# Optimization experiments

Measured on AMD Instinct MI355X. Metric: run time of the kernel, lower is better.

Reference implementation:

```python
import jax, jax.numpy as jnp
import numpy as np


def setup_inputs() -> dict:
    key = jax.random.key(0)
    k1, k2 = jax.random.split(key)
    B, S, D, E = 4, 4096, 2048, 64
    x = jax.random.normal(k1, (B, S, D), dtype=jnp.float32)
    gate_w = jax.random.normal(k2, (E, D), dtype=jnp.float32) * (1.0 / np.sqrt(D))
    return {"x": x, "gate_w": gate_w, "top_k": 2}


def reference(x, gate_w, top_k):
    # logits = x @ W^T : [B, S, E]
    logits = jnp.einsum("bsd,ed->bse", x, gate_w)
    probs = jax.nn.softmax(logits, axis=-1)
    top_k_probs, top_k_indices = jax.lax.top_k(probs, top_k)
    top_k_probs = top_k_probs / jnp.sum(top_k_probs, axis=-1, keepdims=True)
    return (top_k_probs, top_k_indices, probs)
```

## Files before the change

### kernel.cpp

```cpp
#include <hip/hip_runtime.h>
#include <math.h>


typedef _Float16 half8  __attribute__((ext_vector_type(8)));
typedef float    floatx4 __attribute__((ext_vector_type(4)));

#define NTOK  16384
#define DDIM  2048
#define NE    64
#define TPB   64
#define NSTEP 32

__device__ inline void split8(const float4& a, const float4& b,
                              half8& hi, half8& lo) {
    float f[8] = {a.x, a.y, a.z, a.w, b.x, b.y, b.z, b.w};
#pragma unroll
    for (int j = 0; j < 8; ++j) {
        const _Float16 h = (_Float16)f[j];
        hi[j] = h;
        lo[j] = (_Float16)(f[j] - (float)h);
    }
}

__global__ __launch_bounds__(256) void w_split(const float* __restrict__ W,
                                               _Float16* __restrict__ img) {
    const int idx  = blockIdx.x * 256 + threadIdx.x;
    const int step = idx >> 10;
    const int u    = idx & 1023;
    const int hl   = u >> 9;
    const int v    = u & 511;
    const int e    = v >> 3, g = v & 7;
    const float* src = W + (size_t)e * DDIM + step * 64 + 8 * (g ^ (e & 7));
    const float4 a = *(const float4*)(src);
    const float4 b = *(const float4*)(src + 4);
    half8 hi, lo;
    split8(a, b, hi, lo);
    *(half8*)(img + (size_t)idx * 8) = (hl == 0) ? hi : lo;
}

__global__ __launch_bounds__(512) void router_mfma(
    const float* __restrict__ x,
    const _Float16* __restrict__ img,
    float* __restrict__ out)
{
    __shared__ __align__(16) float tiles[16384];
    __shared__ __align__(16) float lg[TPB * 68];

    const int tid = threadIdx.x;
    const int L   = tid & 63;
    const int wv  = __builtin_amdgcn_readfirstlane(tid >> 6);
    const int kh  = wv & 1;
    const int nh  = (wv >> 1) & 1;
    const int mh  = wv >> 2;
    const int c   = L & 15, q = L >> 4;
    const int tok0 = blockIdx.x * TPB;

    const int gfrag = (q + 4 * kh) ^ (L & 7);
    int aoff[2], boff[2];
#pragma unroll
    for (int mt = 0; mt < 2; ++mt)
        aoff[mt] = ((mh * 32 + mt * 16 + c) * 8 + gfrag) * 8;
#pragma unroll
    for (int nt = 0; nt < 2; ++nt)
        boff[nt] = ((nh * 32 + nt * 16 + c) * 8 + gfrag) * 8;

    const int sr = tid >> 3, so = tid & 7;
    const float* xsrc = x + (size_t)(tok0 + sr) * DDIM + 8 * (so ^ (sr & 7));
    const int    xdst = (sr * 8 + so) * 8;
    const float* wsrc = (const float*)img;

    {
        const float4 xa  = *(const float4*)(xsrc);
        const float4 xb  = *(const float4*)(xsrc + 4);
        const float4 wh4 = *(const float4*)(wsrc + (size_t)tid * 4);
        const float4 wl4 = *(const float4*)(wsrc + (size_t)(512 + tid) * 4);
        _Float16* nb = (_Float16*)&tiles[0];
        half8 hi, lo; split8(xa, xb, hi, lo);
        *(half8*)(nb + xdst)        = hi;
        *(half8*)(nb + 4096 + xdst) = lo;
        *(float4*)(nb + 8192  + tid * 8) = wh4;
        *(float4*)(nb + 12288 + tid * 8) = wl4;
    }
    __syncthreads();

    floatx4 acc[2][2];
#pragma unroll
    for (int i = 0; i < 2; ++i)
#pragma unroll
        for (int j = 0; j < 2; ++j) acc[i][j] = (floatx4)0.f;

#pragma unroll 2
    for (int t = 0; t < NSTEP; ++t) {
        float4 xa, xb, wh4, wl4;
        if (t + 1 < NSTEP) {
            xa  = *(const float4*)(xsrc + (t + 1) * 64);
            xb  = *(const float4*)(xsrc + (t + 1) * 64 + 4);
            wh4 = *(const float4*)(wsrc + (size_t)((t + 1) * 1024 + tid) * 4);
            wl4 = *(const float4*)(wsrc + (size_t)((t + 1) * 1024 + 512 + tid) * 4);
        }

        const _Float16* base = (const _Float16*)&tiles[(t & 1) * 8192];
        const _Float16* xh = base;
        const _Float16* xl = base + 4096;
        const _Float16* wh = base + 8192;
        const _Float16* wl = base + 12288;

        half8 Ah[2], Al[2], Bh[2], Bl[2];
#pragma unroll
        for (int mt = 0; mt < 2; ++mt) {
            Ah[mt] = *(const half8*)(xh + aoff[mt]);
            Al[mt] = *(const half8*)(xl + aoff[mt]);
        }
#pragma unroll
        for (int nt = 0; nt < 2; ++nt) {
            Bh[nt] = *(const half8*)(wh + boff[nt]);
            Bl[nt] = *(const half8*)(wl + boff[nt]);
        }
#pragma unroll
        for (int mt = 0; mt < 2; ++mt)
#pragma unroll
            for (int nt = 0; nt < 2; ++nt) {
                acc[mt][nt] = __builtin_amdgcn_mfma_f32_16x16x32_f16(Ah[mt], Bh[nt], acc[mt][nt], 0, 0, 0);
                acc[mt][nt] = __builtin_amdgcn_mfma_f32_16x16x32_f16(Al[mt], Bh[nt], acc[mt][nt], 0, 0, 0);
                acc[mt][nt] = __builtin_amdgcn_mfma_f32_16x16x32_f16(Ah[mt], Bl[nt], acc[mt][nt], 0, 0, 0);
            }

        if (t + 1 < NSTEP) {
            _Float16* nb = (_Float16*)&tiles[((t + 1) & 1) * 8192];
            half8 hi, lo; split8(xa, xb, hi, lo);
            *(half8*)(nb + xdst)        = hi;
            *(half8*)(nb + 4096 + xdst) = lo;
            *(float4*)(nb + 8192  + tid * 8) = wh4;
            *(float4*)(nb + 12288 + tid * 8) = wl4;
        }
        __syncthreads();
    }

    float* exch = tiles;
    const int p = wv >> 1;
    if (kh == 1) {
        float* e0 = &exch[(p * 64 + L) * 20];
        *(float4*)(e0 + 0)  = make_float4(acc[0][0][0], acc[0][0][1], acc[0][0][2], acc[0][0][3]);
        *(float4*)(e0 + 4)  = make_float4(acc[0][1][0], acc[0][1][1], acc[0][1][2], acc[0][1][3]);
        *(float4*)(e0 + 8)  = make_float4(acc[1][0][0], acc[1][0][1], acc[1][0][2], acc[1][0][3]);
        *(float4*)(e0 + 12) = make_float4(acc[1][1][0], acc[1][1][1], acc[1][1][2], acc[1][1][3]);
    }
    __syncthreads();
    if (kh == 0) {
        const float* e0 = &exch[(p * 64 + L) * 20];
        float4 v;
        v = *(const float4*)(e0 + 0);  acc[0][0][0] += v.x; acc[0][0][1] += v.y; acc[0][0][2] += v.z; acc[0][0][3] += v.w;
        v = *(const float4*)(e0 + 4);  acc[0][1][0] += v.x; acc[0][1][1] += v.y; acc[0][1][2] += v.z; acc[0][1][3] += v.w;
        v = *(const float4*)(e0 + 8);  acc[1][0][0] += v.x; acc[1][0][1] += v.y; acc[1][0][2] += v.z; acc[1][0][3] += v.w;
        v = *(const float4*)(e0 + 12); acc[1][1][0] += v.x; acc[1][1][1] += v.y; acc[1][1][2] += v.z; acc[1][1][3] += v.w;
#pragma unroll
        for (int mt = 0; mt < 2; ++mt)
#pragma unroll
            for (int nt = 0; nt < 2; ++nt)
#pragma unroll
                for (int r = 0; r < 4; ++r)
                    lg[(mh * 32 + mt * 16 + q * 4 + r) * 68 + nh * 32 + nt * 16 + c] = acc[mt][nt][r];
    }
    __syncthreads();

    if (tid < 64) {
        const int token = tok0 + tid;
        float* row = &lg[tid * 68];
        float pr[NE];
#pragma unroll
        for (int e = 0; e < NE; ++e) pr[e] = row[e];

        float m = pr[0];
#pragma unroll
        for (int e = 1; e < NE; ++e) m = fmaxf(m, pr[e]);
        float s = 0.f;
#pragma unroll
        for (int e = 0; e < NE; ++e) { pr[e] = expf(pr[e] - m); s += pr[e]; }
        const float inv = 1.f / s;

        float v1 = -1.f; int i1 = 0;
#pragma unroll
        for (int e = 0; e < NE; ++e) { if (pr[e] > v1) { v1 = pr[e]; i1 = e; } }
        float v2 = -1.f; int i2 = 0;
#pragma unroll
        for (int e = 0; e < NE; ++e) { if (e != i1 && pr[e] > v2) { v2 = pr[e]; i2 = e; } }

        const float ts = v1 + v2;
        float* out_tp = out;
        float* out_ti = out + 2 * NTOK;
        *(float2*)(out_tp + token * 2) = make_float2(v1 / ts, v2 / ts);
        *(float2*)(out_ti + token * 2) = make_float2((float)i1, (float)i2);

#pragma unroll
        for (int e = 0; e < NE; ++e) row[e] = pr[e] * inv;
    }
    __syncthreads();

    {
        float* out_p = out + 4 * NTOK + (size_t)tok0 * NE;
#pragma unroll
        for (int i = 0; i < 2; ++i) {
            const int f = tid + 512 * i;
            const int r = f >> 4, c4 = f & 15;
            const float4 v = *(const float4*)&lg[r * 68 + 4 * c4];
            *(float4*)(out_p + f * 4) = v;
        }
    }
}

extern "C" void kernel_launch(void* const* d_in, const int* in_sizes, int n_in,
                              void* d_out, int out_size, void* d_ws, size_t ws_size,
                              hipStream_t stream) {
    const float* x = (const float*)d_in[0];
    const float* W = (const float*)d_in[1];
    float* out     = (float*)d_out;
    _Float16* img  = (_Float16*)d_ws;

    w_split<<<dim3(128), dim3(256), 0, stream>>>(W, img);
    router_mfma<<<dim3(NTOK / TPB), dim3(512), 0, stream>>>(x, img, out);
}
```

Measured before the change: 209.5 us.

## Load MFMA fragments directly from global memory, dropping the LDS staging

The GEMM main loop stops staging x and split W tiles through double-buffered shared memory with a barrier each step. Each wave now loads its x fragments straight from global memory into registers and splits them there. It reads W hi/lo fragments from a new pre-swizzled workspace layout that matches the MFMA operand order, using register double buffering. Blocks shrink to 32 tokens and 256 threads with two waves splitting K, which removes per-step synchronisation but increases register pressure and W re-reads from L2 per block.

New measurement: 226.2 us. 8.0% more time.

```diff
diff --git a/kernel.cpp b/kernel.cpp
--- a/kernel.cpp
+++ b/kernel.cpp
@@ -8,8 +8,6 @@
 #define NTOK  16384
 #define DDIM  2048
 #define NE    64
-#define TPB   64
-#define NSTEP 32
 
 __device__ inline void split8(const float4& a, const float4& b,
                               half8& hi, half8& lo) {
@@ -22,149 +20,110 @@
     }
 }
 
-__global__ __launch_bounds__(256) void w_split(const float* __restrict__ W,
-                                               _Float16* __restrict__ img) {
-    const int idx  = blockIdx.x * 256 + threadIdx.x;
-    const int step = idx >> 10;
-    const int u    = idx & 1023;
-    const int hl   = u >> 9;
-    const int v    = u & 511;
-    const int e    = v >> 3, g = v & 7;
-    const float* src = W + (size_t)e * DDIM + step * 64 + 8 * (g ^ (e & 7));
+__global__ __launch_bounds__(256) void w_split2(const float* __restrict__ W,
+                                                _Float16* __restrict__ img) {
+    const int g  = blockIdx.x * 256 + threadIdx.x;
+    const int L  = g & 63;
+    const int Bk = g >> 6;
+    const int h  = Bk & 1;
+    const int nt = (Bk >> 1) & 3;
+    const int ch = (Bk >> 3) & 1;
+    const int s  = (Bk >> 4) & 15;
+    const int kk = (Bk >> 8) & 1;
+    const int c  = L & 15, q = L >> 4;
+    const float* src = W + (size_t)(nt * 16 + c) * DDIM
+                         + kk * 1024 + s * 64 + ch * 32 + q * 8;
     const float4 a = *(const float4*)(src);
     const float4 b = *(const float4*)(src + 4);
     half8 hi, lo;
     split8(a, b, hi, lo);
-    *(half8*)(img + (size_t)idx * 8) = (hl == 0) ? hi : lo;
+    *(half8*)(img + (size_t)g * 8) = h ? lo : hi;
 }
 
-__global__ __launch_bounds__(512) void router_mfma(
+__global__ __launch_bounds__(256, 2) void router_mfma(
     const float* __restrict__ x,
     const _Float16* __restrict__ img,
     float* __restrict__ out)
 {
-    __shared__ __align__(16) float tiles[16384];
-    __shared__ __align__(16) float lg[TPB * 68];
+    __shared__ __align__(16) float lg[32 * 68];
 
     const int tid = threadIdx.x;
     const int L   = tid & 63;
     const int wv  = __builtin_amdgcn_readfirstlane(tid >> 6);
-    const int kh  = wv & 1;
-    const int nh  = (wv >> 1) & 1;
-    const int mh  = wv >> 2;
+    const int kk  = wv & 1;
+    const int tg  = wv >> 1;
     const int c   = L & 15, q = L >> 4;
-    const int tok0 = blockIdx.x * TPB;
+    const int btok = blockIdx.x * 32;
+    const int tok0 = btok + tg * 16;
 
-    const int gfrag = (q + 4 * kh) ^ (L & 7);
-    int aoff[2], boff[2];
+    const float*    xp = x + (size_t)(tok0 + c) * DDIM + kk * 1024 + q * 8;
+    const _Float16* wp = img + (size_t)kk * 131072 + (size_t)L * 8;
+
+    floatx4 acc[4];
 #pragma unroll
-    for (int mt = 0; mt < 2; ++mt)
-        aoff[mt] = ((mh * 32 + mt * 16 + c) * 8 + gfrag) * 8;
+    for (int nt = 0; nt < 4; ++nt) acc[nt] = (floatx4)0.f;
+
+    float4 xb0[4], xb1[4];
+    half8  wb0[16], wb1[16];
+
+    auto LX = [&](int s, float4* xb) {
 #pragma unroll
-    for (int nt = 0; nt < 2; ++nt)
-        boff[nt] = ((nh * 32 + nt * 16 + c) * 8 + gfrag) * 8;
+        for (int ch = 0; ch < 2; ++ch) {
+            xb[2 * ch + 0] = *(const float4*)(xp + s * 64 + ch * 32);
+            xb[2 * ch + 1] = *(const float4*)(xp + s * 64 + ch * 32 + 4);
+        }
+    };
+    auto LW = [&](int s, half8* wb) {
+#pragma unroll
+        for (int f = 0; f < 16; ++f)
+            wb[f] = *(const half8*)(wp + (size_t)s * 8192 + f * 512);
+    };
+    auto CP = [&](const float4* xb, const half8* wb) {
+#pragma unroll
+        for (int ch = 0; ch < 2; ++ch) {
+            half8 Ah, Al;
+            split8(xb[2 * ch], xb[2 * ch + 1], Ah, Al);
+#pragma unroll
+            for (int nt = 0; nt < 4; ++nt) {
+                const half8 Bh = wb[ch * 8 + nt * 2];
+                const half8 Bl = wb[ch * 8 + nt * 2 + 1];
+                acc[nt] = __builtin_amdgcn_mfma_f32_16x16x32_f16(Ah, Bh, acc[nt], 0, 0, 0);
+                acc[nt] = __builtin_amdgcn_mfma_f32_16x16x32_f16(Al, Bh, acc[nt], 0, 0, 0);
+                acc[nt] = __builtin_amdgcn_mfma_f32_16x16x32_f16(Ah, Bl, acc[nt], 0, 0, 0);
+            }
+        }
+    };
 
-    const int sr = tid >> 3, so = tid & 7;
-    const float* xsrc = x + (size_t)(tok0 + sr) * DDIM + 8 * (so ^ (sr & 7));
-    const int    xdst = (sr * 8 + so) * 8;
-    const float* wsrc = (const float*)img;
+    LX(0, xb0); LW(0, wb0);
+#pragma unroll
+    for (int b = 0; b < 16; b += 2) {
+        LX(b + 1, xb1); LW(b + 1, wb1);
+        CP(xb0, wb0);
+        if (b + 2 < 16) { LX(b + 2, xb0); LW(b + 2, wb0); }
+        CP(xb1, wb1);
+    }
 
-    {
-        const float4 xa  = *(const float4*)(xsrc);
-        const float4 xb  = *(const float4*)(xsrc + 4);
-        const float4 wh4 = *(const float4*)(wsrc + (size_t)tid * 4);
-        const float4 wl4 = *(const float4*)(wsrc + (size_t)(512 + tid) * 4);
-        _Float16* nb = (_Float16*)&tiles[0];
-        half8 hi, lo; split8(xa, xb, hi, lo);
-        *(half8*)(nb + xdst)        = hi;
-        *(half8*)(nb + 4096 + xdst) = lo;
-        *(float4*)(nb + 8192  + tid * 8) = wh4;
-        *(float4*)(nb + 12288 + tid * 8) = wl4;
+    if (kk == 1) {
+#pragma unroll
+        for (int nt = 0; nt < 4; ++nt)
+#pragma unroll
+            for (int r = 0; r < 4; ++r)
+                lg[(tg * 16 + q * 4 + r) * 68 + nt * 16 + c] = acc[nt][r];
+    }
+    __syncthreads();
+    if (kk == 0) {
+#pragma unroll
+        for (int nt = 0; nt < 4; ++nt)
+#pragma unroll
+            for (int r = 0; r < 4; ++r) {
+                const int o = (tg * 16 + q * 4 + r) * 68 + nt * 16 + c;
+                lg[o] += acc[nt][r];
+            }
     }
     __syncthreads();
 
-    floatx4 acc[2][2];
-#pragma unroll
-    for (int i = 0; i < 2; ++i)
-#pragma unroll
-        for (int j = 0; j < 2; ++j) acc[i][j] = (floatx4)0.f;
-
-#pragma unroll 2
-    for (int t = 0; t < NSTEP; ++t) {
-        float4 xa, xb, wh4, wl4;
-        if (t + 1 < NSTEP) {
-            xa  = *(const float4*)(xsrc + (t + 1) * 64);
-            xb  = *(const float4*)(xsrc + (t + 1) * 64 + 4);
-            wh4 = *(const float4*)(wsrc + (size_t)((t + 1) * 1024 + tid) * 4);
-            wl4 = *(const float4*)(wsrc + (size_t)((t + 1) * 1024 + 512 + tid) * 4);
-        }
-
-        const _Float16* base = (const _Float16*)&tiles[(t & 1) * 8192];
-        const _Float16* xh = base;
-        const _Float16* xl = base + 4096;
-        const _Float16* wh = base + 8192;
-        const _Float16* wl = base + 12288;
-
-        half8 Ah[2], Al[2], Bh[2], Bl[2];
-#pragma unroll
-        for (int mt = 0; mt < 2; ++mt) {
-            Ah[mt] = *(const half8*)(xh + aoff[mt]);
-            Al[mt] = *(const half8*)(xl + aoff[mt]);
-        }
-#pragma unroll
-        for (int nt = 0; nt < 2; ++nt) {
-            Bh[nt] = *(const half8*)(wh + boff[nt]);
-            Bl[nt] = *(const half8*)(wl + boff[nt]);
-        }
-#pragma unroll
-        for (int mt = 0; mt < 2; ++mt)
-#pragma unroll
-            for (int nt = 0; nt < 2; ++nt) {
-                acc[mt][nt] = __builtin_amdgcn_mfma_f32_16x16x32_f16(Ah[mt], Bh[nt], acc[mt][nt], 0, 0, 0);
-                acc[mt][nt] = __builtin_amdgcn_mfma_f32_16x16x32_f16(Al[mt], Bh[nt], acc[mt][nt], 0, 0, 0);
-                acc[mt][nt] = __builtin_amdgcn_mfma_f32_16x16x32_f16(Ah[mt], Bl[nt], acc[mt][nt], 0, 0, 0);
-            }
-
-        if (t + 1 < NSTEP) {
-            _Float16* nb = (_Float16*)&tiles[((t + 1) & 1) * 8192];
-            half8 hi, lo; split8(xa, xb, hi, lo);
-            *(half8*)(nb + xdst)        = hi;
-            *(half8*)(nb + 4096 + xdst) = lo;
-            *(float4*)(nb + 8192  + tid * 8) = wh4;
-            *(float4*)(nb + 12288 + tid * 8) = wl4;
-        }
-        __syncthreads();
-    }
-
-    float* exch = tiles;
-    const int p = wv >> 1;
-    if (kh == 1) {
-        float* e0 = &exch[(p * 64 + L) * 20];
-        *(float4*)(e0 + 0)  = make_float4(acc[0][0][0], acc[0][0][1], acc[0][0][2], acc[0][0][3]);
-        *(float4*)(e0 + 4)  = make_float4(acc[0][1][0], acc[0][1][1], acc[0][1][2], acc[0][1][3]);
-        *(float4*)(e0 + 8)  = make_float4(acc[1][0][0], acc[1][0][1], acc[1][0][2], acc[1][0][3]);
-        *(float4*)(e0 + 12) = make_float4(acc[1][1][0], acc[1][1][1], acc[1][1][2], acc[1][1][3]);
-    }
-    __syncthreads();
-    if (kh == 0) {
-        const float* e0 = &exch[(p * 64 + L) * 20];
-        float4 v;
-        v = *(const float4*)(e0 + 0);  acc[0][0][0] += v.x; acc[0][0][1] += v.y; acc[0][0][2] += v.z; acc[0][0][3] += v.w;
-        v = *(const float4*)(e0 + 4);  acc[0][1][0] += v.x; acc[0][1][1] += v.y; acc[0][1][2] += v.z; acc[0][1][3] += v.w;
-        v = *(const float4*)(e0 + 8);  acc[1][0][0] += v.x; acc[1][0][1] += v.y; acc[1][0][2] += v.z; acc[1][0][3] += v.w;
-        v = *(const float4*)(e0 + 12); acc[1][1][0] += v.x; acc[1][1][1] += v.y; acc[1][1][2] += v.z; acc[1][1][3] += v.w;
-#pragma unroll
-        for (int mt = 0; mt < 2; ++mt)
-#pragma unroll
-            for (int nt = 0; nt < 2; ++nt)
-#pragma unroll
-                for (int r = 0; r < 4; ++r)
-                    lg[(mh * 32 + mt * 16 + q * 4 + r) * 68 + nh * 32 + nt * 16 + c] = acc[mt][nt][r];
-    }
-    __syncthreads();
-
-    if (tid < 64) {
-        const int token = tok0 + tid;
+    if (tid < 32) {
+        const int token = btok + tid;
         float* row = &lg[tid * 68];
         float pr[NE];
 #pragma unroll
@@ -197,10 +156,10 @@
     __syncthreads();
 
     {
-        float* out_p = out + 4 * NTOK + (size_t)tok0 * NE;
+        float* out_p = out + 4 * NTOK + (size_t)btok * NE;
 #pragma unroll
         for (int i = 0; i < 2; ++i) {
-            const int f = tid + 512 * i;
+            const int f = tid + 256 * i;
             const int r = f >> 4, c4 = f & 15;
             const float4 v = *(const float4*)&lg[r * 68 + 4 * c4];
             *(float4*)(out_p + f * 4) = v;
@@ -216,6 +175,6 @@
     float* out     = (float*)d_out;
     _Float16* img  = (_Float16*)d_ws;
 
-    w_split<<<dim3(128), dim3(256), 0, stream>>>(W, img);
-    router_mfma<<<dim3(NTOK / TPB), dim3(512), 0, stream>>>(x, img, out);
+    w_split2<<<dim3(128), dim3(256), 0, stream>>>(W, img);
+    router_mfma<<<dim3(NTOK / 32), dim3(256), 0, stream>>>(x, img, out);
 }
```
